# Performance work log

Measured on AMD Instinct MI355X. Metric: run time of the kernel, lower is better.

The kernel has to match this reference:

```python
import jax, jax.numpy as jnp
import numpy as np

N, E, D, H, C, G, L = 100000, 1600000, 128, 4, 32, 4096, 3  # nodes, edges, h_dim, heads, head_dim, graphs, conv blocks


def setup_inputs() -> dict:
    key = jax.random.key(0)
    ks = jax.random.split(key, 24)
    s = 0.05
    w = lambda k, shape: jax.random.normal(k, shape, jnp.float32) * s
    inp = {
        "x": jax.random.normal(ks[0], (N, D), jnp.float32),
        "edge_index": jax.random.randint(ks[1], (2, E), 0, N),
        "batch": jnp.sort(jax.random.randint(ks[2], (N,), 0, G)),
        # input TransformerConv (in=D, out=C per head, H heads, beta=True)
        "in_Wq": w(ks[3], (D, D)), "in_bq": jnp.zeros((D,), jnp.float32),
        "in_Wk": w(ks[4], (D, D)), "in_bk": jnp.zeros((D,), jnp.float32),
        "in_Wv": w(ks[5], (D, D)), "in_bv": jnp.zeros((D,), jnp.float32),
        "in_Ws": w(ks[6], (D, D)), "in_bs": jnp.zeros((D,), jnp.float32),
        "in_Wbeta": w(ks[7], (3 * D,)),
        # stacked conv blocks (L of them, in=out=D)
        "blk_Wq": w(ks[8], (L, D, D)), "blk_bq": jnp.zeros((L, D), jnp.float32),
        "blk_Wk": w(ks[9], (L, D, D)), "blk_bk": jnp.zeros((L, D), jnp.float32),
        "blk_Wv": w(ks[10], (L, D, D)), "blk_bv": jnp.zeros((L, D), jnp.float32),
        "blk_Ws": w(ks[11], (L, D, D)), "blk_bs": jnp.zeros((L, D), jnp.float32),
        "blk_Wbeta": w(ks[12], (L, 3 * D)),
        # MLP head
        "W1": w(ks[13], (D, 64)), "b1": jnp.zeros((64,), jnp.float32),
        "W2": w(ks[14], (64, 32)), "b2": jnp.zeros((32,), jnp.float32),
        "W3": w(ks[15], (32, 1)), "b3": jnp.zeros((1,), jnp.float32),
    }
    return inp


def transformer_conv(x, src, dst, Wq, bq, Wk, bk, Wv, bv, Ws, bs, Wbeta):
    # PyG TransformerConv, concat=True, root_weight=True, beta=True, eval mode
    q = (x @ Wq + bq).reshape(N, H, C)
    k = (x @ Wk + bk).reshape(N, H, C)
    v = (x @ Wv + bv).reshape(N, H, C)
    # per-edge attention logits: message j=src -> i=dst
    alpha = jnp.einsum("ehc,ehc->eh", q[dst], k[src]) / jnp.sqrt(jnp.float32(C))  # [E,H]
    m = jax.ops.segment_max(alpha, dst, num_segments=N)
    m = jnp.where(jnp.isfinite(m), m, 0.0)
    e = jnp.exp(alpha - m[dst])
    denom = jax.ops.segment_sum(e, dst, num_segments=N)
    a = e / (denom[dst] + 1e-16)  # segment softmax over in-edges of dst
    msg = a[..., None] * v[src]  # [E,H,C]
    out = jax.ops.segment_sum(msg, dst, num_segments=N).reshape(N, H * C)
    x_r = x @ Ws + bs
    beta = jax.nn.sigmoid(jnp.concatenate([out, x_r, out - x_r], axis=-1) @ Wbeta)[:, None]
    return beta * x_r + (1.0 - beta) * out


def reference(x, edge_index, batch, in_Wq, in_bq, in_Wk, in_bk, in_Wv, in_bv,
              in_Ws, in_bs, in_Wbeta, blk_Wq, blk_bq, blk_Wk, blk_bk, blk_Wv,
              blk_bv, blk_Ws, blk_bs, blk_Wbeta, W1, b1, W2, b2, W3, b3):
    src, dst = edge_index[0], edge_index[1]
    h = jax.nn.relu(transformer_conv(x, src, dst, in_Wq, in_bq, in_Wk, in_bk,
                                     in_Wv, in_bv, in_Ws, in_bs, in_Wbeta))
    for l in range(L):  # dropout is identity in eval mode
        h = jax.nn.relu(transformer_conv(h, src, dst, blk_Wq[l], blk_bq[l],
                                         blk_Wk[l], blk_bk[l], blk_Wv[l], blk_bv[l],
                                         blk_Ws[l], blk_bs[l], blk_Wbeta[l]))
    # global mean pool over graphs
    sums = jax.ops.segment_sum(h, batch, num_segments=G)
    cnt = jax.ops.segment_sum(jnp.ones((N, 1), h.dtype), batch, num_segments=G)
    g = sums / jnp.maximum(cnt, 1.0)
    g = jax.nn.relu(g @ W1 + b1)
    g = jax.nn.relu(g @ W2 + b2)
    return jax.nn.sigmoid(g @ W3 + b3)
```

## Files before the change

kernel.cpp:

```cpp
#include <hip/hip_runtime.h>
#include <hip/hip_bf16.h>
#include <cstdint>

#define DH 128
#define NB 256
#define NBK 1024

typedef __attribute__((ext_vector_type(8))) short short8;
typedef __attribute__((ext_vector_type(4))) float floatx4;
typedef __attribute__((ext_vector_type(2))) float floatx2;

__device__ __forceinline__ float bflo(unsigned u) { return __uint_as_float(u << 16); }
__device__ __forceinline__ float bfhi(unsigned u) { return __uint_as_float(u & 0xffff0000u); }

__device__ __forceinline__ unsigned pk_bf16(float a, float b) {
  return ((unsigned)__bfloat16_as_ushort(__float2bfloat16(b)) << 16)
       | (unsigned)__bfloat16_as_ushort(__float2bfloat16(a));
}

template<int CTRL>
__device__ __forceinline__ float dpp_add(float x) {
  int y = __builtin_amdgcn_update_dpp(0, __float_as_int(x), CTRL, 0xf, 0xf, true);
  return x + __int_as_float(y);
}


__global__ void cvt_bf16(const float* __restrict__ x, __hip_bfloat16* __restrict__ o, int n) {
  int i = blockIdx.x * 256 + threadIdx.x;
  if (i < n) o[i] = __float2bfloat16(x[i]);
}


__global__ void scan1_kernel(const int* __restrict__ deg, int* __restrict__ off,
                             int* __restrict__ bsum, int n) {
  __shared__ int sh[256];
  int idx = blockIdx.x * 256 + threadIdx.x;
  int v = (idx < n) ? deg[idx] : 0;
  sh[threadIdx.x] = v;
  __syncthreads();
  for (int d = 1; d < 256; d <<= 1) {
    int x = (threadIdx.x >= (unsigned)d) ? sh[threadIdx.x - d] : 0;
    __syncthreads();
    sh[threadIdx.x] += x;
    __syncthreads();
  }
  if (idx < n) off[idx] = sh[threadIdx.x] - v;
  if (threadIdx.x == 255) bsum[blockIdx.x] = sh[255];
}

__global__ void scan2_kernel(int* __restrict__ bsum, int nb) {
  __shared__ int sh[512];
  int t = threadIdx.x;
  int v = (t < nb) ? bsum[t] : 0;
  sh[t] = v;
  __syncthreads();
  for (int d = 1; d < 512; d <<= 1) {
    int x = (t >= (unsigned)d) ? sh[t - d] : 0;
    __syncthreads();
    sh[t] += x;
    __syncthreads();
  }
  if (t < nb) bsum[t] = sh[t] - v;
}

__global__ void scan3_kernel(int* __restrict__ off, const int* __restrict__ bsum, int n) {
  int idx = blockIdx.x * 256 + threadIdx.x;
  if (idx < n) off[idx] += bsum[blockIdx.x];
}


__global__ __launch_bounds__(256)
void csr_p1(const int* __restrict__ dst, int* __restrict__ hist, int E, int chunk) {
  __shared__ int cnt[NBK];
  const int blk = blockIdx.x, tid = threadIdx.x;
  for (int c = tid; c < NBK; c += 256) cnt[c] = 0;
  __syncthreads();
  int base = blk * chunk;
  int end = base + chunk; if (end > E) end = E;
  for (int e = base + tid; e < end; e += 256) atomicAdd(&cnt[dst[e] >> 7], 1);
  __syncthreads();
  for (int c = tid; c < NBK; c += 256) hist[c * NB + blk] = cnt[c];
}


__global__ __launch_bounds__(256)
void csr_p2(int* __restrict__ hist, int* __restrict__ total) {
  int b = blockIdx.x * 4 + (threadIdx.x >> 6);
  int lane = threadIdx.x & 63;
  int4 v = *(int4*)&hist[b * NB + lane * 4];
  int s0 = v.x;
  int s1 = s0 + v.y;
  int s2 = s1 + v.z;
  int s3 = s2 + v.w;
  int t = s3;
  for (int d = 1; d < 64; d <<= 1) {
    int y = __shfl_up(t, d);
    if (lane >= d) t += y;
  }
  int excl = t - s3;
  int4 o;
  o.x = excl; o.y = excl + s0; o.z = excl + s1; o.w = excl + s2;
  *(int4*)&hist[b * NB + lane * 4] = o;
  if (lane == 63) total[b] = t;
}

__global__ __launch_bounds__(256)
void csr_p3(const int* __restrict__ src, const int* __restrict__ dst,
            const int* __restrict__ hist, const int* __restrict__ tstart,
            int* __restrict__ part, int E, int chunk) {
  __shared__ int cur[NBK];
  const int blk = blockIdx.x, tid = threadIdx.x;
  for (int c = tid; c < NBK; c += 256) cur[c] = hist[c * NB + blk] + tstart[c];
  __syncthreads();
  int base = blk * chunk;
  int end = base + chunk; if (end > E) end = E;
  for (int e = base + tid; e < end; e += 256) {
    int d = dst[e];
    int b = d >> 7;
    int pos = atomicAdd(&cur[b], 1);
    part[pos] = (src[e] << 7) | (d & 127);
  }
}

__global__ __launch_bounds__(256)
void csr_p4(const int* __restrict__ part, const int* __restrict__ tstart,
            const int* __restrict__ total, int* __restrict__ deg,
            int* __restrict__ off, int* __restrict__ csr, int Nn) {
  __shared__ int lcnt[128], lscan[128], lcur[128];
  const int b = blockIdx.x, tid = threadIdx.x;
  const int p0 = tstart[b];
  const int m = total[b];
  if (tid < 128) lcnt[tid] = 0;
  __syncthreads();
  for (int k = tid; k < m; k += 256) atomicAdd(&lcnt[part[p0 + k] & 127], 1);
  __syncthreads();
  if (tid < 128) lscan[tid] = lcnt[tid];
  __syncthreads();
  for (int d = 1; d < 128; d <<= 1) {
    int v = 0;
    if (tid < 128 && tid >= d) v = lscan[tid - d];
    __syncthreads();
    if (tid < 128) lscan[tid] += v;
    __syncthreads();
  }
  if (tid < 128) {
    int ex = lscan[tid] - lcnt[tid];
    lcur[tid] = ex;
    int n = (b << 7) + tid;
    if (n < Nn) { deg[n] = lcnt[tid]; off[n] = p0 + ex; }
  }
  __syncthreads();
  for (int k = tid; k < m; k += 256) {
    int pk = part[p0 + k];
    int pos = p0 + atomicAdd(&lcur[pk & 127], 1);
    csr[pos] = pk >> 7;
  }
}


__global__ void goff_kernel(const int* __restrict__ batch, int* __restrict__ goff,
                            int N, int G) {
  int g = blockIdx.x * 256 + threadIdx.x;
  if (g > G) return;
  if (g == G) { goff[G] = N; return; }
  int lo = 0, hi = N;
  while (lo < hi) { int mid = (lo + hi) >> 1; if (batch[mid] < g) lo = mid + 1; else hi = mid; }
  goff[g] = lo;
}


__global__ __launch_bounds__(256)
void pack_w_kernel(const float* __restrict__ Wq, const float* __restrict__ Wk,
                   const float* __restrict__ Wv, const float* __restrict__ Ws,
                   const float* __restrict__ bq, const float* __restrict__ bk,
                   const float* __restrict__ bv, const float* __restrict__ bs,
                   __hip_bfloat16* __restrict__ WT2, float* __restrict__ bcat) {
  if (blockIdx.x == 64) {
    for (int c = threadIdx.x; c < 512; c += 256) {
      int which = c >> 7, cc = c & 127;
      const float* b = (which == 0) ? bq : (which == 1) ? bk : (which == 2) ? bv : bs;
      bcat[c] = b[cc];
    }
    return;
  }
  __shared__ float tile[32][33];
  const int bid = blockIdx.x;
  const int which = bid >> 4, kb = (bid >> 2) & 3, cb = bid & 3;
  const float* W = (which == 0) ? Wq : (which == 1) ? Wk : (which == 2) ? Wv : Ws;
  const int tx = threadIdx.x & 31, ty = threadIdx.x >> 5;
#pragma unroll
  for (int r = ty; r < 32; r += 8)
    tile[r][tx] = W[(kb * 32 + r) * 128 + cb * 32 + tx];
  __syncthreads();
  const int t = threadIdx.x;
  const int mt_sel = t >> 7;
  const int s4 = (t & 127) * 4;
  const int l16 = s4 >> 5;
  const int quad = (s4 >> 3) & 3;
  const int j0 = s4 & 7;
  const int cl = mt_sel * 16 + l16;
  const int kr = quad * 8 + j0;
  float f0 = tile[kr + 0][cl];
  float f1 = tile[kr + 1][cl];
  float f2 = tile[kr + 2][cl];
  float f3 = tile[kr + 3][cl];
  const int mt = which * 8 + cb * 2 + mt_sel;
  const int o = mt * 2048 + kb * 512 + l16 * 32 + quad * 8 + j0;
  uint2 w;
  w.x = pk_bf16(f0, f1);
  w.y = pk_bf16(f2, f3);
  *(uint2*)&((unsigned short*)WT2)[o] = w;
}


__global__ __launch_bounds__(256)
void gemm_qkvs(const short* __restrict__ Xb, const short* __restrict__ WT2,
               const float* __restrict__ bc,
               unsigned int* __restrict__ qout,
               unsigned int* __restrict__ kvp,
               unsigned int* __restrict__ xrout, int Nn) {
  __shared__ short As[64][132];
  const int row0 = blockIdx.x * 64;
  const int tid = threadIdx.x;

#pragma unroll
  for (int p = 0; p < 4; ++p) {
    int chunk = p * 256 + tid;
    int r = chunk >> 4, c8 = chunk & 15;
    int row = row0 + r; if (row >= Nn) row = Nn - 1;
    *(int4*)&As[r][c8 * 8] = *(const int4*)&Xb[(size_t)row * 128 + c8 * 8];
  }
  __syncthreads();

  const int w = tid >> 6, lane = tid & 63, quad = lane >> 4, l16 = lane & 15;

  short8 xf[4][4];
#pragma unroll
  for (int nt = 0; nt < 4; ++nt)
#pragma unroll
    for (int kt = 0; kt < 4; ++kt)
      xf[nt][kt] = *(const short8*)&As[nt * 16 + l16][kt * 32 + quad * 8];

  const int fbase = l16 * 32 + quad * 8;

  if (w == 0 || w == 3) {
    unsigned int* outp = (w == 0) ? qout : xrout;
    const int mbase = (w == 0) ? 0 : 24;
#pragma unroll
    for (int i = 0; i < 8; ++i) {
      const int mt = mbase + i;
      short8 af[4];
#pragma unroll
      for (int kt = 0; kt < 4; ++kt)
        af[kt] = *(const short8*)&WT2[mt * 2048 + kt * 512 + fbase];
      float4 bias = *(const float4*)&bc[mt * 16 + quad * 4];
      const int wc = (i * 16 + quad * 4);
#pragma unroll
      for (int nt = 0; nt < 4; ++nt) {
        floatx4 acc = (floatx4){0.f, 0.f, 0.f, 0.f};
#pragma unroll
        for (int kt = 0; kt < 4; ++kt)
          acc = __builtin_amdgcn_mfma_f32_16x16x32_bf16(af[kt], xf[nt][kt], acc, 0, 0, 0);
        int node = row0 + nt * 16 + l16;
        if (node < Nn) {
          uint2 o;
          o.x = pk_bf16(acc[0] + bias.x, acc[1] + bias.y);
          o.y = pk_bf16(acc[2] + bias.z, acc[3] + bias.w);
          *(uint2*)&outp[(size_t)node * 64 + (wc >> 1)] = o;
        }
      }
    }
  } else {
    const int kb = 8 + (w - 1) * 4;
    const int vb = 16 + (w - 1) * 4;
#pragma unroll
    for (int i = 0; i < 4; ++i) {
      const int mk = kb + i, mv = vb + i;
      short8 afk[4], afv[4];
#pragma unroll
      for (int kt = 0; kt < 4; ++kt) {
        afk[kt] = *(const short8*)&WT2[mk * 2048 + kt * 512 + fbase];
        afv[kt] = *(const short8*)&WT2[mv * 2048 + kt * 512 + fbase];
      }
      float4 bk4 = *(const float4*)&bc[mk * 16 + quad * 4];
      float4 bv4 = *(const float4*)&bc[mv * 16 + quad * 4];
      const int krel = (w - 1) * 64 + i * 16 + quad * 4;
#pragma unroll
      for (int nt = 0; nt < 4; ++nt) {
        floatx4 ak = (floatx4){0.f, 0.f, 0.f, 0.f};
        floatx4 av = (floatx4){0.f, 0.f, 0.f, 0.f};
#pragma unroll
        for (int kt = 0; kt < 4; ++kt) {
          ak = __builtin_amdgcn_mfma_f32_16x16x32_bf16(afk[kt], xf[nt][kt], ak, 0, 0, 0);
          av = __builtin_amdgcn_mfma_f32_16x16x32_bf16(afv[kt], xf[nt][kt], av, 0, 0, 0);
        }
        int node = row0 + nt * 16 + l16;
        if (node < Nn) {
          int d0 = __builtin_amdgcn_cvt_pk_fp8_f32(ak[0] + bk4.x, ak[1] + bk4.y, 0, false);
          d0 = __builtin_amdgcn_cvt_pk_fp8_f32(av[0] + bv4.x, av[1] + bv4.y, d0, true);
          int d1 = __builtin_amdgcn_cvt_pk_fp8_f32(ak[2] + bk4.z, ak[3] + bk4.w, 0, false);
          d1 = __builtin_amdgcn_cvt_pk_fp8_f32(av[2] + bv4.z, av[3] + bv4.w, d1, true);
          uint2 o; o.x = (unsigned)d0; o.y = (unsigned)d1;
          *(uint2*)&kvp[(size_t)node * 64 + (krel >> 1)] = o;
        }
      }
    }
  }
}


__global__ __launch_bounds__(256)
void attn_kernel(unsigned int* __restrict__ q_h, const uint2* __restrict__ kvp2,
                 const uint2* __restrict__ xr2, const int* __restrict__ off,
                 const int* __restrict__ deg, const int* __restrict__ csr,
                 const float* __restrict__ Wb, int Nn) {
  int wv = __builtin_amdgcn_readfirstlane(threadIdx.x >> 6);
  int i = blockIdx.x * 4 + wv;
  if (i >= Nn) return;
  const int l = threadIdx.x & 63;
  const int j = l & 31;
  const int g = l >> 5;

  const float QS = 0.17677669529663687f * 1.4426950408889634f;
  uint2 qw = ((const uint2*)q_h)[(size_t)i * 32 + j];
  float q0 = bflo(qw.x) * QS, q1 = bfhi(qw.x) * QS;
  float q2 = bflo(qw.y) * QS, q3 = bfhi(qw.y) * QS;

  const int e0 = off[i];
  const int dg = deg[i];

  float denA = 0.f, aA0 = 0.f, aA1 = 0.f, aA2 = 0.f, aA3 = 0.f;
  float denB = 0.f, aB0 = 0.f, aB1 = 0.f, aB2 = 0.f, aB3 = 0.f;

  auto pair = [&](int s0, int s1, float& den, float& a0, float& a1, float& a2, float& a3) {
    int s = g ? s1 : s0;
    uint2 kv = kvp2[(unsigned)((s << 5) | j)];
    floatx2 k01 = __builtin_amdgcn_cvt_pk_f32_fp8((int)kv.x, false);
    floatx2 v01 = __builtin_amdgcn_cvt_pk_f32_fp8((int)kv.x, true);
    floatx2 k23 = __builtin_amdgcn_cvt_pk_f32_fp8((int)kv.y, false);
    floatx2 v23 = __builtin_amdgcn_cvt_pk_f32_fp8((int)kv.y, true);
    float d = q0 * k01.x + q1 * k01.y + q2 * k23.x + q3 * k23.y;
    d = dpp_add<0xB1>(d);
    d = dpp_add<0x4E>(d);
    d += __shfl_xor(d, 4);
    float p = exp2f(d);
    den += p;
    a0 += p * v01.x; a1 += p * v01.y; a2 += p * v23.x; a3 += p * v23.y;
  };

  const int nPair = dg >> 1;
  int e = e0;
  int it = 0;
  for (; it + 1 < nPair; it += 2) {
    int s0 = csr[e], s1 = csr[e + 1], s2 = csr[e + 2], s3 = csr[e + 3];
    pair(s0, s1, denA, aA0, aA1, aA2, aA3);
    pair(s2, s3, denB, aB0, aB1, aB2, aB3);
    e += 4;
  }
  if (it < nPair) {
    int s0 = csr[e], s1 = csr[e + 1];
    pair(s0, s1, denA, aA0, aA1, aA2, aA3);
    e += 2;
  }
  if (dg & 1) {
    int s0 = csr[e];
    int s = s0;
    uint2 kv = kvp2[(unsigned)((s << 5) | j)];
    floatx2 k01 = __builtin_amdgcn_cvt_pk_f32_fp8((int)kv.x, false);
    floatx2 v01 = __builtin_amdgcn_cvt_pk_f32_fp8((int)kv.x, true);
    floatx2 k23 = __builtin_amdgcn_cvt_pk_f32_fp8((int)kv.y, false);
    floatx2 v23 = __builtin_amdgcn_cvt_pk_f32_fp8((int)kv.y, true);
    float d = q0 * k01.x + q1 * k01.y + q2 * k23.x + q3 * k23.y;
    d = dpp_add<0xB1>(d);
    d = dpp_add<0x4E>(d);
    d += __shfl_xor(d, 4);
    float p = (g == 0) ? exp2f(d) : 0.f;
    denB += p;
    aB0 += p * v01.x; aB1 += p * v01.y; aB2 += p * v23.x; aB3 += p * v23.y;
  }

  float den = denA + denB;
  float a0 = aA0 + aB0, a1 = aA1 + aB1, a2 = aA2 + aB2, a3 = aA3 + aB3;
  den += __shfl_xor(den, 32);
  a0 += __shfl_xor(a0, 32);
  a1 += __shfl_xor(a1, 32);
  a2 += __shfl_xor(a2, 32);
  a3 += __shfl_xor(a3, 32);
  float inv = 1.f / (den + 1e-16f);
  float o0 = a0 * inv, o1 = a1 * inv, o2 = a2 * inv, o3 = a3 * inv;

  uint2 xw = xr2[(size_t)i * 32 + j];
  float xr0 = bflo(xw.x), xr1 = bfhi(xw.x);
  float xr2v = bflo(xw.y), xr3 = bfhi(xw.y);

  float4 wo = *(const float4*)&Wb[4 * j];
  float4 wx = *(const float4*)&Wb[128 + 4 * j];
  float4 wd = *(const float4*)&Wb[256 + 4 * j];
  float c = o0 * wo.x + o1 * wo.y + o2 * wo.z + o3 * wo.w
          + xr0 * wx.x + xr1 * wx.y + xr2v * wx.z + xr3 * wx.w
          + (o0 - xr0) * wd.x + (o1 - xr1) * wd.y + (o2 - xr2v) * wd.z + (o3 - xr3) * wd.w;
  c += __shfl_xor(c, 1);
  c += __shfl_xor(c, 2);
  c += __shfl_xor(c, 4);
  c += __shfl_xor(c, 8);
  c += __shfl_xor(c, 16);
  float beta = 1.f / (1.f + __expf(-c));

  if (g == 0) {
    float h0 = fmaxf(beta * xr0 + (1.f - beta) * o0, 0.f);
    float h1 = fmaxf(beta * xr1 + (1.f - beta) * o1, 0.f);
    float h2 = fmaxf(beta * xr2v + (1.f - beta) * o2, 0.f);
    float h3 = fmaxf(beta * xr3 + (1.f - beta) * o3, 0.f);
    uint2 hw;
    hw.x = pk_bf16(h0, h1);
    hw.y = pk_bf16(h2, h3);
    ((uint2*)q_h)[(size_t)i * 32 + j] = hw;
  }
}


__global__ __launch_bounds__(128)
void poolmlp_kernel(const unsigned short* __restrict__ h, const int* __restrict__ goff,
                    const float* __restrict__ W1, const float* __restrict__ b1,
                    const float* __restrict__ W2, const float* __restrict__ b2,
                    const float* __restrict__ W3, const float* __restrict__ b3,
                    float* __restrict__ out) {
  int g = blockIdx.x;
  int t = threadIdx.x;
  int n0 = goff[g], cnt = goff[g + 1] - n0;
  float s = 0.f;
  for (int n = n0; n < n0 + cnt; ++n) s += bflo(h[(size_t)n * 128 + t]);
  __shared__ float gv[128];
  __shared__ float t1[64];
  __shared__ float t2[32];
  gv[t] = s / fmaxf((float)cnt, 1.0f);
  __syncthreads();
  if (t < 64) {
    float a = b1[t];
    for (int k = 0; k < 128; ++k) a += gv[k] * W1[k * 64 + t];
    t1[t] = fmaxf(a, 0.f);
  }
  __syncthreads();
  if (t < 32) {
    float a = b2[t];
    for (int k = 0; k < 64; ++k) a += t1[k] * W2[k * 32 + t];
    t2[t] = fmaxf(a, 0.f);
  }
  __syncthreads();
  if (t == 0) {
    float a = b3[0];
    for (int k = 0; k < 32; ++k) a += t2[k] * W3[k];
    out[g] = 1.f / (1.f + __expf(-a));
  }
}


extern "C" void kernel_launch(void* const* d_in, const int* in_sizes, int n_in,
                              void* d_out, int out_size, void* d_ws, size_t ws_size,
                              hipStream_t stream) {
  const float* x = (const float*)d_in[0];
  const int* edge_index = (const int*)d_in[1];
  const int* batch = (const int*)d_in[2];
  const int N = in_sizes[0] / DH;
  const int E = in_sizes[1] / 2;
  const int G = out_size;
  const int* src = edge_index;
  const int* dst = edge_index + E;

  const float* in_Wq = (const float*)d_in[3];
  const float* in_bq = (const float*)d_in[4];
  const float* in_Wk = (const float*)d_in[5];
  const float* in_bk = (const float*)d_in[6];
  const float* in_Wv = (const float*)d_in[7];
  const float* in_bv = (const float*)d_in[8];
  const float* in_Ws = (const float*)d_in[9];
  const float* in_bs = (const float*)d_in[10];
  const float* in_Wbeta = (const float*)d_in[11];
  const float* blk_Wq = (const float*)d_in[12];
  const float* blk_bq = (const float*)d_in[13];
  const float* blk_Wk = (const float*)d_in[14];
  const float* blk_bk = (const float*)d_in[15];
  const float* blk_Wv = (const float*)d_in[16];
  const float* blk_bv = (const float*)d_in[17];
  const float* blk_Ws = (const float*)d_in[18];
  const float* blk_bs = (const float*)d_in[19];
  const float* blk_Wbeta = (const float*)d_in[20];

  char* p = (char*)d_ws;
  auto take = [&](size_t bytes) { char* r = p; p += (bytes + 255) & ~(size_t)255; return r; };
  __hip_bfloat16* h0 = (__hip_bfloat16*)take((size_t)N * DH * 2);
  __hip_bfloat16* h1 = (__hip_bfloat16*)take((size_t)N * DH * 2);
  unsigned char* kvp = (unsigned char*)take((size_t)N * 256);
  unsigned short* xr = (unsigned short*)take((size_t)N * DH * 2);
  __hip_bfloat16* WT2 = (__hip_bfloat16*)take((size_t)512 * DH * 2);
  float* bcat = (float*)take(512 * 4);
  int* deg    = (int*)take((size_t)N * 4);
  int* off    = (int*)take((size_t)N * 4);
  int* csr    = (int*)take((size_t)E * 4);
  int* part   = (int*)take((size_t)E * 4);
  int* hist   = (int*)take((size_t)NB * NBK * 4);
  int* total  = (int*)take(NBK * 4);
  int* tstart = (int*)take(NBK * 4);
  int* bsumP  = (int*)take(512 * 4);
  int* goff   = (int*)take((size_t)(G + 1) * 4);
  (void)n_in;
  if ((size_t)(p - (char*)d_ws) > ws_size) return;

  const int NBUCK = (N + 127) >> 7;
  const int chunk = (E + NB - 1) / NB;

  csr_p1<<<NB, 256, 0, stream>>>(dst, hist, E, chunk);
  csr_p2<<<NBK / 4, 256, 0, stream>>>(hist, total);
  scan1_kernel<<<NBK / 256, 256, 0, stream>>>(total, tstart, bsumP, NBK);
  scan2_kernel<<<1, 512, 0, stream>>>(bsumP, NBK / 256);
  scan3_kernel<<<NBK / 256, 256, 0, stream>>>(tstart, bsumP, NBK);
  csr_p3<<<NB, 256, 0, stream>>>(src, dst, hist, tstart, part, E, chunk);
  csr_p4<<<NBUCK, 256, 0, stream>>>(part, tstart, total, deg, off, csr, N);

  goff_kernel<<<(G + 256) / 256, 256, 0, stream>>>(batch, goff, N, G);

  cvt_bf16<<<(int)(((size_t)N * DH + 255) / 256), 256, 0, stream>>>(x, h0, N * DH);

  for (int l = 0; l < 4; ++l) {
    const float *Wq, *Wk, *Wv, *Ws, *bq, *bk, *bv, *bs, *Wb;
    if (l == 0) {
      Wq = in_Wq; Wk = in_Wk; Wv = in_Wv; Ws = in_Ws;
      bq = in_bq; bk = in_bk; bv = in_bv; bs = in_bs; Wb = in_Wbeta;
    } else {
      int m = l - 1;
      Wq = blk_Wq + (size_t)m * DH * DH; Wk = blk_Wk + (size_t)m * DH * DH;
      Wv = blk_Wv + (size_t)m * DH * DH; Ws = blk_Ws + (size_t)m * DH * DH;
      bq = blk_bq + (size_t)m * DH; bk = blk_bk + (size_t)m * DH;
      bv = blk_bv + (size_t)m * DH; bs = blk_bs + (size_t)m * DH;
      Wb = blk_Wbeta + (size_t)m * 3 * DH;
    }
    __hip_bfloat16* hin  = (l & 1) ? h1 : h0;
    __hip_bfloat16* qbuf = (l & 1) ? h0 : h1;
    pack_w_kernel<<<65, 256, 0, stream>>>(Wq, Wk, Wv, Ws, bq, bk, bv, bs, WT2, bcat);
    gemm_qkvs<<<(N + 63) / 64, 256, 0, stream>>>((const short*)hin, (const short*)WT2, bcat,
        (unsigned int*)qbuf, (unsigned int*)kvp, (unsigned int*)xr, N);
    attn_kernel<<<(N + 3) / 4, 256, 0, stream>>>((unsigned int*)qbuf, (const uint2*)kvp,
        (const uint2*)xr, off, deg, csr, Wb, N);
  }

  poolmlp_kernel<<<G, 128, 0, stream>>>((const unsigned short*)h0, goff,
      (const float*)d_in[21], (const float*)d_in[22],
      (const float*)d_in[23], (const float*)d_in[24],
      (const float*)d_in[25], (const float*)d_in[26],
      (float*)d_out);
}
```

Before: 725.6 us.

## Fuse attention of each layer with next layer's QKVS GEMM via shared-memory tile

The attention output for 64 nodes per block is written to shared memory as bf16 and fed directly into the next layer's QKV/skip MFMA GEMM, removing the global h write and re-read between layers. The first GEMM converts the fp32 input in its load loop, which drops the separate cvt_bf16 kernel. All four weight packs are hoisted ahead of the chain, and q/kv/xr buffers are double-buffered so the fused kernel can read layer l while writing layer l+1. The cost is that each block now runs attention for 16 nodes per wave serially before the GEMM, so latency hiding within a block is lower and occupancy may change.

```diff
diff --git a/kernel.cpp b/kernel.cpp
--- a/kernel.cpp
+++ b/kernel.cpp
@@ -22,12 +22,6 @@
 __device__ __forceinline__ float dpp_add(float x) {
   int y = __builtin_amdgcn_update_dpp(0, __float_as_int(x), CTRL, 0xf, 0xf, true);
   return x + __int_as_float(y);
-}
-
-
-__global__ void cvt_bf16(const float* __restrict__ x, __hip_bfloat16* __restrict__ o, int n) {
-  int i = blockIdx.x * 256 + threadIdx.x;
-  if (i < n) o[i] = __float2bfloat16(x[i]);
 }
 
 
@@ -81,7 +75,6 @@
   __syncthreads();
   for (int c = tid; c < NBK; c += 256) hist[c * NB + blk] = cnt[c];
 }
-
 
 __global__ __launch_bounds__(256)
 void csr_p2(int* __restrict__ hist, int* __restrict__ total) {
@@ -213,25 +206,11 @@
 }
 
 
-__global__ __launch_bounds__(256)
-void gemm_qkvs(const short* __restrict__ Xb, const short* __restrict__ WT2,
-               const float* __restrict__ bc,
-               unsigned int* __restrict__ qout,
-               unsigned int* __restrict__ kvp,
-               unsigned int* __restrict__ xrout, int Nn) {
-  __shared__ short As[64][132];
-  const int row0 = blockIdx.x * 64;
-  const int tid = threadIdx.x;
-
-#pragma unroll
-  for (int p = 0; p < 4; ++p) {
-    int chunk = p * 256 + tid;
-    int r = chunk >> 4, c8 = chunk & 15;
-    int row = row0 + r; if (row >= Nn) row = Nn - 1;
-    *(int4*)&As[r][c8 * 8] = *(const int4*)&Xb[(size_t)row * 128 + c8 * 8];
-  }
-  __syncthreads();
-
+__device__ __forceinline__ void gemm_phase(
+    const short* __restrict__ WT2, const float* __restrict__ bc,
+    unsigned int* __restrict__ qout, unsigned int* __restrict__ kvp,
+    unsigned int* __restrict__ xrout, int Nn, int row0, int tid,
+    const short (*As)[132]) {
   const int w = tid >> 6, lane = tid & 63, quad = lane >> 4, l16 = lane & 15;
 
   short8 xf[4][4];
@@ -309,20 +288,14 @@
 }
 
 
-__global__ __launch_bounds__(256)
-void attn_kernel(unsigned int* __restrict__ q_h, const uint2* __restrict__ kvp2,
-                 const uint2* __restrict__ xr2, const int* __restrict__ off,
-                 const int* __restrict__ deg, const int* __restrict__ csr,
-                 const float* __restrict__ Wb, int Nn) {
-  int wv = __builtin_amdgcn_readfirstlane(threadIdx.x >> 6);
-  int i = blockIdx.x * 4 + wv;
-  if (i >= Nn) return;
-  const int l = threadIdx.x & 63;
-  const int j = l & 31;
-  const int g = l >> 5;
-
+__device__ __forceinline__ uint2 attn_node(
+    int i, int j, int g,
+    const uint2* __restrict__ qbuf, const uint2* __restrict__ kvp2,
+    const uint2* __restrict__ xr2, const int* __restrict__ off,
+    const int* __restrict__ deg, const int* __restrict__ csr,
+    const float* __restrict__ Wb) {
   const float QS = 0.17677669529663687f * 1.4426950408889634f;
-  uint2 qw = ((const uint2*)q_h)[(size_t)i * 32 + j];
+  uint2 qw = qbuf[(size_t)i * 32 + j];
   float q0 = bflo(qw.x) * QS, q1 = bfhi(qw.x) * QS;
   float q2 = bflo(qw.y) * QS, q3 = bfhi(qw.y) * QS;
 
@@ -363,8 +336,7 @@
     e += 2;
   }
   if (dg & 1) {
-    int s0 = csr[e];
-    int s = s0;
+    int s = csr[e];
     uint2 kv = kvp2[(unsigned)((s << 5) | j)];
     floatx2 k01 = __builtin_amdgcn_cvt_pk_f32_fp8((int)kv.x, false);
     floatx2 v01 = __builtin_amdgcn_cvt_pk_f32_fp8((int)kv.x, true);
@@ -406,16 +378,80 @@
   c += __shfl_xor(c, 16);
   float beta = 1.f / (1.f + __expf(-c));
 
-  if (g == 0) {
-    float h0 = fmaxf(beta * xr0 + (1.f - beta) * o0, 0.f);
-    float h1 = fmaxf(beta * xr1 + (1.f - beta) * o1, 0.f);
-    float h2 = fmaxf(beta * xr2v + (1.f - beta) * o2, 0.f);
-    float h3 = fmaxf(beta * xr3 + (1.f - beta) * o3, 0.f);
-    uint2 hw;
-    hw.x = pk_bf16(h0, h1);
-    hw.y = pk_bf16(h2, h3);
-    ((uint2*)q_h)[(size_t)i * 32 + j] = hw;
-  }
+  float h0 = fmaxf(beta * xr0 + (1.f - beta) * o0, 0.f);
+  float h1 = fmaxf(beta * xr1 + (1.f - beta) * o1, 0.f);
+  float h2 = fmaxf(beta * xr2v + (1.f - beta) * o2, 0.f);
+  float h3 = fmaxf(beta * xr3 + (1.f - beta) * o3, 0.f);
+  uint2 hw;
+  hw.x = pk_bf16(h0, h1);
+  hw.y = pk_bf16(h2, h3);
+  return hw;
+}
+
+
+__global__ __launch_bounds__(256)
+void gemm0_kernel(const float* __restrict__ Xf, const short* __restrict__ WT2,
+                  const float* __restrict__ bc,
+                  unsigned int* __restrict__ qout, unsigned int* __restrict__ kvp,
+                  unsigned int* __restrict__ xrout, int Nn) {
+  __shared__ short As[64][132];
+  const int row0 = blockIdx.x * 64;
+  const int tid = threadIdx.x;
+#pragma unroll
+  for (int p = 0; p < 8; ++p) {
+    int chunk = p * 256 + tid;
+    int r = chunk >> 5;
+    int c4 = (chunk & 31) * 4;
+    int row = row0 + r; if (row >= Nn) row = Nn - 1;
+    float4 f = *(const float4*)&Xf[(size_t)row * 128 + c4];
+    uint2 pk;
+    pk.x = pk_bf16(f.x, f.y);
+    pk.y = pk_bf16(f.z, f.w);
+    *(uint2*)&As[r][c4] = pk;
+  }
+  __syncthreads();
+  gemm_phase(WT2, bc, qout, kvp, xrout, Nn, row0, tid, As);
+}
+
+
+__global__ __launch_bounds__(256)
+void attn_gemm_kernel(const uint2* __restrict__ qb, const uint2* __restrict__ kvpl,
+                      const uint2* __restrict__ xrl, const int* __restrict__ off,
+                      const int* __restrict__ deg, const int* __restrict__ csr,
+                      const float* __restrict__ Wb,
+                      const short* __restrict__ WT2n, const float* __restrict__ bcn,
+                      unsigned int* __restrict__ qo, unsigned int* __restrict__ kvpn,
+                      unsigned int* __restrict__ xro, int Nn) {
+  __shared__ short As[64][132];
+  const int tid = threadIdx.x;
+  const int row0 = blockIdx.x * 64;
+  const int w = __builtin_amdgcn_readfirstlane(tid >> 6);
+  const int l = tid & 63;
+  const int j = l & 31, g = l >> 5;
+
+  for (int r = 0; r < 16; ++r) {
+    int i = row0 + w * 16 + r;
+    uint2 hw; hw.x = 0u; hw.y = 0u;
+    if (i < Nn) hw = attn_node(i, j, g, qb, kvpl, xrl, off, deg, csr, Wb);
+    if (g == 0) *(uint2*)&As[w * 16 + r][4 * j] = hw;
+  }
+  __syncthreads();
+  gemm_phase(WT2n, bcn, qo, kvpn, xro, Nn, row0, tid, As);
+}
+
+
+__global__ __launch_bounds__(256)
+void attn_final_kernel(unsigned int* __restrict__ q_h, const uint2* __restrict__ kvp2,
+                       const uint2* __restrict__ xr2, const int* __restrict__ off,
+                       const int* __restrict__ deg, const int* __restrict__ csr,
+                       const float* __restrict__ Wb, int Nn) {
+  int wv = __builtin_amdgcn_readfirstlane(threadIdx.x >> 6);
+  int i = blockIdx.x * 4 + wv;
+  if (i >= Nn) return;
+  const int l = threadIdx.x & 63;
+  const int j = l & 31, g = l >> 5;
+  uint2 hw = attn_node(i, j, g, (const uint2*)q_h, kvp2, xr2, off, deg, csr, Wb);
+  if (g == 0) ((uint2*)q_h)[(size_t)i * 32 + j] = hw;
 }
 
 
@@ -488,12 +524,14 @@
 
   char* p = (char*)d_ws;
   auto take = [&](size_t bytes) { char* r = p; p += (bytes + 255) & ~(size_t)255; return r; };
-  __hip_bfloat16* h0 = (__hip_bfloat16*)take((size_t)N * DH * 2);
-  __hip_bfloat16* h1 = (__hip_bfloat16*)take((size_t)N * DH * 2);
-  unsigned char* kvp = (unsigned char*)take((size_t)N * 256);
-  unsigned short* xr = (unsigned short*)take((size_t)N * DH * 2);
-  __hip_bfloat16* WT2 = (__hip_bfloat16*)take((size_t)512 * DH * 2);
-  float* bcat = (float*)take(512 * 4);
+  unsigned* qA = (unsigned*)take((size_t)N * DH * 2);
+  unsigned* qB = (unsigned*)take((size_t)N * DH * 2);
+  unsigned char* kvpA = (unsigned char*)take((size_t)N * 256);
+  unsigned char* kvpB = (unsigned char*)take((size_t)N * 256);
+  unsigned* xrA = (unsigned*)take((size_t)N * DH * 2);
+  unsigned* xrB = (unsigned*)take((size_t)N * DH * 2);
+  __hip_bfloat16* WT2 = (__hip_bfloat16*)take((size_t)4 * 512 * DH * 2);
+  float* bcat = (float*)take((size_t)4 * 512 * 4);
   int* deg    = (int*)take((size_t)N * 4);
   int* off    = (int*)take((size_t)N * 4);
   int* csr    = (int*)take((size_t)E * 4);
@@ -508,6 +546,7 @@
 
   const int NBUCK = (N + 127) >> 7;
   const int chunk = (E + NB - 1) / NB;
+  const int NGB = (N + 63) / 64;
 
   csr_p1<<<NB, 256, 0, stream>>>(dst, hist, E, chunk);
   csr_p2<<<NBK / 4, 256, 0, stream>>>(hist, total);
@@ -519,31 +558,45 @@
 
   goff_kernel<<<(G + 256) / 256, 256, 0, stream>>>(batch, goff, N, G);
 
-  cvt_bf16<<<(int)(((size_t)N * DH + 255) / 256), 256, 0, stream>>>(x, h0, N * DH);
-
   for (int l = 0; l < 4; ++l) {
-    const float *Wq, *Wk, *Wv, *Ws, *bq, *bk, *bv, *bs, *Wb;
+    const float *Wq, *Wk, *Wv, *Ws, *bq, *bk, *bv, *bs;
     if (l == 0) {
       Wq = in_Wq; Wk = in_Wk; Wv = in_Wv; Ws = in_Ws;
-      bq = in_bq; bk = in_bk; bv = in_bv; bs = in_bs; Wb = in_Wbeta;
+      bq = in_bq; bk = in_bk; bv = in_bv; bs = in_bs;
     } else {
       int m = l - 1;
       Wq = blk_Wq + (size_t)m * DH * DH; Wk = blk_Wk + (size_t)m * DH * DH;
       Wv = blk_Wv + (size_t)m * DH * DH; Ws = blk_Ws + (size_t)m * DH * DH;
       bq = blk_bq + (size_t)m * DH; bk = blk_bk + (size_t)m * DH;
       bv = blk_bv + (size_t)m * DH; bs = blk_bs + (size_t)m * DH;
-      Wb = blk_Wbeta + (size_t)m * 3 * DH;
     }
-    __hip_bfloat16* hin  = (l & 1) ? h1 : h0;
-    __hip_bfloat16* qbuf = (l & 1) ? h0 : h1;
-    pack_w_kernel<<<65, 256, 0, stream>>>(Wq, Wk, Wv, Ws, bq, bk, bv, bs, WT2, bcat);
-    gemm_qkvs<<<(N + 63) / 64, 256, 0, stream>>>((const short*)hin, (const short*)WT2, bcat,
-        (unsigned int*)qbuf, (unsigned int*)kvp, (unsigned int*)xr, N);
-    attn_kernel<<<(N + 3) / 4, 256, 0, stream>>>((unsigned int*)qbuf, (const uint2*)kvp,
-        (const uint2*)xr, off, deg, csr, Wb, N);
-  }
-
-  poolmlp_kernel<<<G, 128, 0, stream>>>((const unsigned short*)h0, goff,
+    pack_w_kernel<<<65, 256, 0, stream>>>(Wq, Wk, Wv, Ws, bq, bk, bv, bs,
+                                          WT2 + (size_t)l * 512 * DH, bcat + l * 512);
+  }
+
+  const float* Wb0 = in_Wbeta;
+  const float* Wb1 = blk_Wbeta;
+  const float* Wb2 = blk_Wbeta + 384;
+  const float* Wb3 = blk_Wbeta + 768;
+  const short* W0 = (const short*)WT2;
+  const short* W1 = (const short*)(WT2 + (size_t)1 * 512 * DH);
+  const short* W2 = (const short*)(WT2 + (size_t)2 * 512 * DH);
+  const short* W3 = (const short*)(WT2 + (size_t)3 * 512 * DH);
+
+  gemm0_kernel<<<NGB, 256, 0, stream>>>(x, W0, bcat, qA, (unsigned*)kvpA, xrA, N);
+  attn_gemm_kernel<<<NGB, 256, 0, stream>>>((const uint2*)qA, (const uint2*)kvpA,
+      (const uint2*)xrA, off, deg, csr, Wb0, W1, bcat + 512,
+      qB, (unsigned*)kvpB, xrB, N);
+  attn_gemm_kernel<<<NGB, 256, 0, stream>>>((const uint2*)qB, (const uint2*)kvpB,
+      (const uint2*)xrB, off, deg, csr, Wb1, W2, bcat + 1024,
+      qA, (unsigned*)kvpA, xrA, N);
+  attn_gemm_kernel<<<NGB, 256, 0, stream>>>((const uint2*)qA, (const uint2*)kvpA,
+      (const uint2*)xrA, off, deg, csr, Wb2, W3, bcat + 1536,
+      qB, (unsigned*)kvpB, xrB, N);
+  attn_final_kernel<<<(N + 3) / 4, 256, 0, stream>>>(qB, (const uint2*)kvpB,
+      (const uint2*)xrB, off, deg, csr, Wb3, N);
+
+  poolmlp_kernel<<<G, 128, 0, stream>>>((const unsigned short*)qB, goff,
       (const float*)d_in[21], (const float*)d_in[22],
       (const float*)d_in[23], (const float*)d_in[24],
       (const float*)d_in[25], (const float*)d_in[26],
```

Result: slower. 972.7 us (+34.1%).
